# Kernel optimization log

Hardware: AMD Instinct MI355X
Metric: run time of the kernel (lower is better)

The kernel has to match this reference:

```python
import jax, jax.numpy as jnp
import numpy as np

T = 1.0        # temperature t from __init__
THRESH = 0.3   # hard-negative margin from forward
B, D, C, P, N = 64, 256, 100000, 8, 32


def setup_inputs():
    key = jax.random.key(0)
    k1, k2, k3, k4, k5, k6, k7 = jax.random.split(key, 7)
    inputs = jax.random.normal(k1, (B, D), jnp.float32)
    V = jax.random.normal(k2, (C, D), jnp.float32) * 0.05  # memory bank (buffer)
    targets = jax.random.randint(k3, (B,), 0, C)
    pos_idx = jax.random.randint(k4, (B, P), 0, B)
    neg_idx = jax.random.randint(k5, (B, N), 0, B)
    pos_mask = jax.random.randint(k6, (B, P), 0, 2).at[:, 0].set(1)  # >=1 positive
    neg_mask = jax.random.randint(k7, (B, N), 0, 2)
    return {"inputs": inputs, "V": V, "targets": targets,
            "pos_idx": pos_idx, "pos_mask": pos_mask,
            "neg_idx": neg_idx, "neg_mask": neg_mask}


def _forward(inputs, V, targets, pos_idx, pos_mask, neg_idx, neg_mask):
    # Exclusive.forward: inputs @ V.T, scaled by t
    logits = (inputs @ V.T) * T                       # [B, C]
    logp = jax.nn.log_softmax(logits, axis=-1)
    bu_loss = -jnp.mean(jnp.take_along_axis(logp, targets[:, None], axis=1))

    # cosine similarity among batch samples
    nrm = jnp.maximum(jnp.linalg.norm(inputs, axis=1, keepdims=True), 1e-12)
    ni = inputs / nrm
    sim = ni @ ni.T                                   # [B, B]

    rows = jnp.arange(B)[:, None]
    # hardest positive: min similarity over valid positive pairs
    psims = sim[rows, pos_idx]                        # [B, P]
    pm = pos_mask.astype(bool)
    hpsims = jnp.min(jnp.where(pm, psims, jnp.inf), axis=1)   # [B]
    hp_loss = jax.nn.softplus(-hpsims)                # BCE-with-logits vs target 1

    # hard negatives: those with sim > (hardest_pos - 0.3)
    nsims = sim[rows, neg_idx]                        # [B, N]
    sel = neg_mask.astype(bool) & (nsims > (hpsims - THRESH)[:, None])
    cnt = jnp.sum(sel, axis=1)
    hn_sum = jnp.sum(jnp.where(sel, jax.nn.softplus(nsims), 0.0), axis=1)
    hn_loss = jnp.where(cnt > 0, hn_sum / jnp.maximum(cnt, 1), 0.0)

    h_loss = jnp.mean(hp_loss + hn_loss)
    return bu_loss + h_loss, logits


def reference(inputs, V, targets, pos_idx, pos_mask, neg_idx, neg_mask):
    return _forward(inputs, V, targets, pos_idx, pos_mask, neg_idx, neg_mask)
```

## Files before the change

kernel.cpp:

```cpp
#include <hip/hip_runtime.h>
#include <hip/hip_bf16.h>
#include <math.h>

#define B_DIM 64
#define D_DIM 256
#define C_DIM 100000
#define P_DIM 8
#define N_DIM 32
#define BLK_COLS 64
#define GBLK 1563
#define NCHUNK 8
#define NBANK 64

typedef __attribute__((ext_vector_type(8))) short bf16x8;
typedef __attribute__((ext_vector_type(16))) float f32x16;

__device__ __forceinline__ unsigned short bf16_rn(float f) {
    unsigned int u = __float_as_uint(f);
    unsigned int r = (u + 0x7FFFu + ((u >> 16) & 1u)) >> 16;
    return (unsigned short)r;
}

__device__ __forceinline__ void split_bf16(float x, unsigned short& hi, unsigned short& lo) {
    unsigned int bx = __float_as_uint(x);
    unsigned int hb = bx & 0xFFFF0000u;
    hi = (unsigned short)(hb >> 16);
    lo = bf16_rn(x - __uint_as_float(hb));
}

__device__ __forceinline__ float softplusf(float x) { return log1pf(expf(x)); }

__device__ __forceinline__ short f2bf(float x) {
    __hip_bfloat16 b = __float2bfloat16(x);
    return *reinterpret_cast<short*>(&b);
}

__device__ __forceinline__ void async_copy16(const float* src, float* lds_base) {
    __builtin_amdgcn_global_load_lds(
        (const __attribute__((address_space(1))) unsigned int*)src,
        (__attribute__((address_space(3))) unsigned int*)lds_base,
        16, 0, 0);
}

__global__ __launch_bounds__(512)
void prep_kernel(const float* __restrict__ X,
                 const int* __restrict__ pos_idx, const int* __restrict__ pos_mask,
                 const int* __restrict__ neg_idx, const int* __restrict__ neg_mask,
                 float* __restrict__ wsH, unsigned short* __restrict__ wsA,
                 float* __restrict__ wsQ, float* __restrict__ wsT) {
    __shared__ unsigned short fHi[2048 * 8];
    __shared__ unsigned short fLo[2048 * 8];
    __shared__ float sim[64][64];
    __shared__ float inv[64];
    __shared__ float hp[64];
    __shared__ float contrib[64];
    const int tid = threadIdx.x;
    for (int i = tid; i < NBANK * 64; i += 512) wsQ[i] = 0.0f;
    if (tid < 64) wsT[tid] = 0.0f;
    if (tid < 256) {
        int r = tid >> 2, q = tid & 3;
        const float* row = X + r * D_DIM + q * 64;
        float s = 0.0f;
        #pragma unroll
        for (int i = 0; i < 64; i += 4) {
            float4 v = *(const float4*)(row + i);
            s += v.x * v.x + v.y * v.y + v.z * v.z + v.w * v.w;
        }
        s += __shfl_xor(s, 1);
        s += __shfl_xor(s, 2);
        if (q == 0) inv[r] = 1.0f / fmaxf(sqrtf(s), 1e-12f);
    }
    __syncthreads();
    for (int t = tid; t < 2048; t += 512) {
        int l = t & 63, kg = (t >> 6) & 15, mt = t >> 10;
        int row = mt * 32 + (l & 31);
        int col0 = kg * 16 + 8 * (l >> 5);
        const float* src = X + row * D_DIM + col0;
        float iv = inv[row];
        #pragma unroll
        for (int j = 0; j < 8; ++j) {
            unsigned short h, lo;
            split_bf16(src[j] * iv, h, lo);
            fHi[t * 8 + j] = h;
            fLo[t * 8 + j] = lo;
            wsA[t * 8 + j] = (unsigned short)f2bf(src[j]);
        }
    }
    __syncthreads();
    if ((tid >> 6) < 4) {
        int w = tid >> 6, l = tid & 63;
        int mt = w >> 1, nt = w & 1;
        f32x16 acc;
        #pragma unroll
        for (int i = 0; i < 16; ++i) acc[i] = 0.0f;
        #pragma unroll
        for (int ks = 0; ks < 16; ++ks) {
            const bf16x8 ah = *(const bf16x8*)&fHi[((mt * 16 + ks) * 64 + l) * 8];
            const bf16x8 al = *(const bf16x8*)&fLo[((mt * 16 + ks) * 64 + l) * 8];
            const bf16x8 bh = *(const bf16x8*)&fHi[((nt * 16 + ks) * 64 + l) * 8];
            const bf16x8 bl = *(const bf16x8*)&fLo[((nt * 16 + ks) * 64 + l) * 8];
            acc = __builtin_amdgcn_mfma_f32_32x32x16_bf16(ah, bh, acc, 0, 0, 0);
            acc = __builtin_amdgcn_mfma_f32_32x32x16_bf16(al, bh, acc, 0, 0, 0);
            acc = __builtin_amdgcn_mfma_f32_32x32x16_bf16(ah, bl, acc, 0, 0, 0);
        }
        #pragma unroll
        for (int r = 0; r < 16; ++r) {
            int brow = mt * 32 + (r & 3) + 8 * (r >> 2) + 4 * (l >> 5);
            int bcol = nt * 32 + (l & 31);
            sim[brow][bcol] = acc[r];
        }
    }
    __syncthreads();
    if (tid < 256) {
        int r = tid >> 2, q = tid & 3;
        const float INF = __int_as_float(0x7f800000);
        float m = INF;
        #pragma unroll
        for (int pp = 0; pp < 2; ++pp) {
            int p = q * 2 + pp;
            int j = pos_idx[r * P_DIM + p];
            int msk = pos_mask[r * P_DIM + p];
            float ps = sim[r][j];
            m = fminf(m, msk ? ps : INF);
        }
        m = fminf(m, __shfl_xor(m, 1));
        m = fminf(m, __shfl_xor(m, 2));
        if (q == 0) hp[r] = m;
    }
    __syncthreads();
    if (tid < 256) {
        int r = tid >> 2, q = tid & 3;
        float thr = hp[r] - 0.3f;
        float sum = 0.0f; int cnt = 0;
        #pragma unroll
        for (int nn = 0; nn < 8; ++nn) {
            int n = q * 8 + nn;
            int j = neg_idx[r * N_DIM + n];
            int msk = neg_mask[r * N_DIM + n];
            float ns = sim[r][j];
            if (msk && (ns > thr)) { cnt += 1; sum += softplusf(ns); }
        }
        sum += __shfl_xor(sum, 1); cnt += __shfl_xor(cnt, 1);
        sum += __shfl_xor(sum, 2); cnt += __shfl_xor(cnt, 2);
        if (q == 0) {
            float hn = (cnt > 0) ? (sum / (float)cnt) : 0.0f;
            contrib[r] = softplusf(-hp[r]) + hn;
        }
    }
    __syncthreads();
    if (tid == 0) {
        float s = 0.0f;
        for (int i = 0; i < 64; ++i) s += contrib[i];
        wsH[0] = s * (1.0f / 64.0f);
    }
}

__global__ __launch_bounds__(128)
void logits_kernel(const float* __restrict__ V, const unsigned short* __restrict__ wsA,
                   const int* __restrict__ targets, float* __restrict__ out,
                   float* __restrict__ wsQ, float* __restrict__ wsT) {
    __shared__ float shm[4352];
    __shared__ int tgt[64];
    const int tid = threadIdx.x;
    const int w = tid >> 6, l = tid & 63;
    const int c0 = blockIdx.x * BLK_COLS;
    const int hi = l >> 5;
    if (tid < 64) tgt[tid] = targets[tid];

    #define STAGE(kc, b)                                                        \
        {                                                                       \
            _Pragma("unroll")                                                   \
            for (int j = 0; j < 4; ++j) {                                       \
                int U = (j * 2 + w) * 64 + l;                                   \
                int colL = U >> 3, up = U & 7;                                  \
                int us = up ^ (colL & 7);                                       \
                int cc = c0 + colL; cc = (cc < C_DIM) ? cc : (C_DIM - 1);       \
                const float* src = V + (size_t)cc * D_DIM + (kc) * 32 + us * 4; \
                async_copy16(src, &shm[(b) * 2048 + (j * 2 + w) * 256]);        \
            }                                                                   \
        }

    STAGE(0, 0);
    __syncthreads();

    f32x16 acc0, acc1;
    #pragma unroll
    for (int i = 0; i < 16; ++i) { acc0[i] = 0.0f; acc1[i] = 0.0f; }

    const int colL = w * 32 + (l & 31);
    const int cbase = colL * 32;
    const int cm7 = colL & 7;

    for (int kc = 0; kc < NCHUNK; ++kc) {
        if (kc < NCHUNK - 1) STAGE(kc + 1, (kc + 1) & 1);
        const float* vb = &shm[(kc & 1) * 2048];
        #pragma unroll
        for (int h = 0; h < 2; ++h) {
            const int kg = kc * 2 + h;
            const bf16x8 a0 = *(const bf16x8*)(wsA + ((0 * 16 + kg) * 64 + l) * 8);
            const bf16x8 a1 = *(const bf16x8*)(wsA + ((1 * 16 + kg) * 64 + l) * 8);
            const int u0 = h * 4 + 2 * hi;
            float4 v0 = *(const float4*)&vb[cbase + ((u0    ) ^ cm7) * 4];
            float4 v1 = *(const float4*)&vb[cbase + ((u0 + 1) ^ cm7) * 4];
            bf16x8 vh;
            vh[0] = f2bf(v0.x); vh[1] = f2bf(v0.y); vh[2] = f2bf(v0.z); vh[3] = f2bf(v0.w);
            vh[4] = f2bf(v1.x); vh[5] = f2bf(v1.y); vh[6] = f2bf(v1.z); vh[7] = f2bf(v1.w);
            acc0 = __builtin_amdgcn_mfma_f32_32x32x16_bf16(vh, a0, acc0, 0, 0, 0);
            acc1 = __builtin_amdgcn_mfma_f32_32x32x16_bf16(vh, a1, acc1, 0, 0, 0);
        }
        __syncthreads();
    }
    #undef STAGE

    float* ldsT = &shm[w * 2112];
    float* sred = &shm[4224];
    const int b0 = l & 31, b1 = 32 + (l & 31);
    const int tb0 = tgt[b0], tb1 = tgt[b1];
    float s0 = 0.0f, s1 = 0.0f;
    #pragma unroll
    for (int r = 0; r < 16; ++r) {
        const int cl = (r & 3) + 8 * (r >> 2) + 4 * hi;
        const int c = c0 + w * 32 + cl;
        const float v0 = acc0[r], v1 = acc1[r];
        ldsT[b0 * 33 + cl] = v0;
        ldsT[b1 * 33 + cl] = v1;
        if (c < C_DIM) {
            s0 += expf(v0);
            s1 += expf(v1);
            if (c == tb0) atomicAdd(&wsT[b0], v0);
            if (c == tb1) atomicAdd(&wsT[b1], v1);
        }
    }
    s0 += __shfl_xor(s0, 32);
    s1 += __shfl_xor(s1, 32);
    if (l < 32) { sred[w * 64 + l] = s0; sred[w * 64 + 32 + l] = s1; }
    __syncthreads();
    if (tid < 64) {
        float s = sred[tid] + sred[64 + tid];
        atomicAdd(&wsQ[(blockIdx.x & (NBANK - 1)) * 64 + tid], s);
    }
    const int cg = c0 + w * 32 + (l & 31);
    if (cg < C_DIM) {
        #pragma unroll
        for (int rr = 0; rr < 32; ++rr) {
            const int b = 2 * rr + hi;
            out[1 + (size_t)b * C_DIM + cg] = ldsT[b * 33 + (l & 31)];
        }
    }
}

__global__ __launch_bounds__(64)
void final_kernel(float* __restrict__ out, const float* __restrict__ wsQ,
                  const float* __restrict__ wsT, const float* __restrict__ wsH) {
    int b = threadIdx.x;
    float S = 0.0f;
    #pragma unroll
    for (int k = 0; k < NBANK; ++k) S += wsQ[k * 64 + b];
    float lb = logf(S) - wsT[b];
    #pragma unroll
    for (int m = 1; m <= 32; m <<= 1) lb += __shfl_xor(lb, m);
    if (b == 0) out[0] = lb * (1.0f / 64.0f) + wsH[0];
}

extern "C" void kernel_launch(void* const* d_in, const int* in_sizes, int n_in,
                              void* d_out, int out_size, void* d_ws, size_t ws_size,
                              hipStream_t stream) {
    (void)in_sizes; (void)n_in; (void)out_size; (void)ws_size;
    const float* X        = (const float*)d_in[0];
    const float* V        = (const float*)d_in[1];
    const int*   targets  = (const int*)d_in[2];
    const int*   pos_idx  = (const int*)d_in[3];
    const int*   pos_mask = (const int*)d_in[4];
    const int*   neg_idx  = (const int*)d_in[5];
    const int*   neg_mask = (const int*)d_in[6];
    float* out = (float*)d_out;
    float*          wsH = (float*)d_ws;
    float*          wsQ = (float*)d_ws + 64;
    float*          wsT = (float*)d_ws + 64 + NBANK * 64;
    unsigned short* wsA = (unsigned short*)((char*)d_ws + 32768);

    hipLaunchKernelGGL(prep_kernel, dim3(1), dim3(512), 0, stream,
                       X, pos_idx, pos_mask, neg_idx, neg_mask, wsH, wsA, wsQ, wsT);
    hipLaunchKernelGGL(logits_kernel, dim3(GBLK), dim3(128), 0, stream,
                       V, wsA, targets, out, wsQ, wsT);
    hipLaunchKernelGGL(final_kernel, dim3(1), dim3(64), 0, stream, out, wsQ, wsT, wsH);
}
```

Baseline: 43.36 us.

## Split logits block across four waves and preload A fragments into registers

The logits kernel now runs 256 threads per block. Each of four waves owns one 32x32 output tile (one of two column halves times one of two batch halves) instead of two waves each computing both batch halves. Each wave preloads its 16 bf16 input fragments into registers once, rather than reloading them from global memory on every k-step, and the k loop is fully unrolled. The staging, transpose and store paths are re-indexed for four waves. This adds latency hiding and removes repeated A loads, at the cost of more register pressure, and each V column is now converted to bf16 by two waves.

```diff
diff --git a/kernel.cpp b/kernel.cpp
--- a/kernel.cpp
+++ b/kernel.cpp
@@ -155,7 +155,7 @@
     }
 }
 
-__global__ __launch_bounds__(128)
+__global__ __launch_bounds__(256)
 void logits_kernel(const float* __restrict__ V, const unsigned short* __restrict__ wsA,
                    const int* __restrict__ targets, float* __restrict__ out,
                    float* __restrict__ wsQ, float* __restrict__ wsT) {
@@ -163,88 +163,88 @@
     __shared__ int tgt[64];
     const int tid = threadIdx.x;
     const int w = tid >> 6, l = tid & 63;
+    const int wc = w & 1, wr = w >> 1;
     const int c0 = blockIdx.x * BLK_COLS;
     const int hi = l >> 5;
     if (tid < 64) tgt[tid] = targets[tid];
 
+    bf16x8 frg[16];
+    #pragma unroll
+    for (int kg = 0; kg < 16; ++kg)
+        frg[kg] = *(const bf16x8*)(wsA + ((wr * 16 + kg) * 64 + l) * 8);
+
     #define STAGE(kc, b)                                                        \
         {                                                                       \
             _Pragma("unroll")                                                   \
-            for (int j = 0; j < 4; ++j) {                                       \
-                int U = (j * 2 + w) * 64 + l;                                   \
+            for (int j = 0; j < 2; ++j) {                                       \
+                int U = (j * 4 + w) * 64 + l;                                   \
                 int colL = U >> 3, up = U & 7;                                  \
                 int us = up ^ (colL & 7);                                       \
                 int cc = c0 + colL; cc = (cc < C_DIM) ? cc : (C_DIM - 1);       \
                 const float* src = V + (size_t)cc * D_DIM + (kc) * 32 + us * 4; \
-                async_copy16(src, &shm[(b) * 2048 + (j * 2 + w) * 256]);        \
+                async_copy16(src, &shm[(b) * 2048 + (j * 4 + w) * 256]);        \
             }                                                                   \
         }
 
     STAGE(0, 0);
     __syncthreads();
 
-    f32x16 acc0, acc1;
-    #pragma unroll
-    for (int i = 0; i < 16; ++i) { acc0[i] = 0.0f; acc1[i] = 0.0f; }
-
-    const int colL = w * 32 + (l & 31);
+    f32x16 acc;
+    #pragma unroll
+    for (int i = 0; i < 16; ++i) acc[i] = 0.0f;
+
+    const int colL = wc * 32 + (l & 31);
     const int cbase = colL * 32;
     const int cm7 = colL & 7;
 
+    #pragma unroll
     for (int kc = 0; kc < NCHUNK; ++kc) {
         if (kc < NCHUNK - 1) STAGE(kc + 1, (kc + 1) & 1);
         const float* vb = &shm[(kc & 1) * 2048];
         #pragma unroll
         for (int h = 0; h < 2; ++h) {
-            const int kg = kc * 2 + h;
-            const bf16x8 a0 = *(const bf16x8*)(wsA + ((0 * 16 + kg) * 64 + l) * 8);
-            const bf16x8 a1 = *(const bf16x8*)(wsA + ((1 * 16 + kg) * 64 + l) * 8);
             const int u0 = h * 4 + 2 * hi;
             float4 v0 = *(const float4*)&vb[cbase + ((u0    ) ^ cm7) * 4];
             float4 v1 = *(const float4*)&vb[cbase + ((u0 + 1) ^ cm7) * 4];
             bf16x8 vh;
             vh[0] = f2bf(v0.x); vh[1] = f2bf(v0.y); vh[2] = f2bf(v0.z); vh[3] = f2bf(v0.w);
             vh[4] = f2bf(v1.x); vh[5] = f2bf(v1.y); vh[6] = f2bf(v1.z); vh[7] = f2bf(v1.w);
-            acc0 = __builtin_amdgcn_mfma_f32_32x32x16_bf16(vh, a0, acc0, 0, 0, 0);
-            acc1 = __builtin_amdgcn_mfma_f32_32x32x16_bf16(vh, a1, acc1, 0, 0, 0);
+            acc = __builtin_amdgcn_mfma_f32_32x32x16_bf16(vh, frg[kc * 2 + h], acc, 0, 0, 0);
         }
         __syncthreads();
     }
     #undef STAGE
 
-    float* ldsT = &shm[w * 2112];
-    float* sred = &shm[4224];
-    const int b0 = l & 31, b1 = 32 + (l & 31);
-    const int tb0 = tgt[b0], tb1 = tgt[b1];
-    float s0 = 0.0f, s1 = 0.0f;
+    float* ldsT = shm;
+    float* sred = &shm[4160];
+    const int b = wr * 32 + (l & 31);
+    const int tb = tgt[b];
+    float s = 0.0f;
     #pragma unroll
     for (int r = 0; r < 16; ++r) {
         const int cl = (r & 3) + 8 * (r >> 2) + 4 * hi;
-        const int c = c0 + w * 32 + cl;
-        const float v0 = acc0[r], v1 = acc1[r];
-        ldsT[b0 * 33 + cl] = v0;
-        ldsT[b1 * 33 + cl] = v1;
+        const int c = c0 + wc * 32 + cl;
+        const float v = acc[r];
+        ldsT[b * 65 + wc * 32 + cl] = v;
         if (c < C_DIM) {
-            s0 += expf(v0);
-            s1 += expf(v1);
-            if (c == tb0) atomicAdd(&wsT[b0], v0);
-            if (c == tb1) atomicAdd(&wsT[b1], v1);
-        }
-    }
-    s0 += __shfl_xor(s0, 32);
-    s1 += __shfl_xor(s1, 32);
-    if (l < 32) { sred[w * 64 + l] = s0; sred[w * 64 + 32 + l] = s1; }
+            s += expf(v);
+            if (c == tb) atomicAdd(&wsT[b], v);
+        }
+    }
+    s += __shfl_xor(s, 32);
+    if (l < 32) sred[w * 32 + l] = s;
     __syncthreads();
     if (tid < 64) {
-        float s = sred[tid] + sred[64 + tid];
-        atomicAdd(&wsQ[(blockIdx.x & (NBANK - 1)) * 64 + tid], s);
-    }
-    const int cg = c0 + w * 32 + (l & 31);
+        const int rw = (tid >> 5) * 2;
+        float t = sred[rw * 32 + (tid & 31)] + sred[(rw + 1) * 32 + (tid & 31)];
+        atomicAdd(&wsQ[(blockIdx.x & (NBANK - 1)) * 64 + tid], t);
+    }
+    const int cg = c0 + l;
     if (cg < C_DIM) {
         #pragma unroll
-        for (int rr = 0; rr < 32; ++rr) {
-            const int b = 2 * rr + hi;
-            out[1 + (size_t)b * C_DIM + cg] = ldsT[b * 33 + (l & 31)];
+        for (int rr = 0; rr < 16; ++rr) {
+            const int bb = rr * 4 + w;
+            out[1 + (size_t)bb * C_DIM + cg] = ldsT[bb * 65 + l];
         }
     }
 }
@@ -281,7 +281,7 @@
 
     hipLaunchKernelGGL(prep_kernel, dim3(1), dim3(512), 0, stream,
                        X, pos_idx, pos_mask, neg_idx, neg_mask, wsH, wsA, wsQ, wsT);
-    hipLaunchKernelGGL(logits_kernel, dim3(GBLK), dim3(128), 0, stream,
+    hipLaunchKernelGGL(logits_kernel, dim3(GBLK), dim3(256), 0, stream,
                        V, wsA, targets, out, wsQ, wsT);
     hipLaunchKernelGGL(final_kernel, dim3(1), dim3(64), 0, stream, out, wsQ, wsT, wsH);
 }
```

New measurement: 46.03 us. 6.2% more time.
